# Optimization experiments

Hardware: AMD Instinct MI355X
Metric: run time of the kernel (lower is better)

## Reference

```python
import jax, jax.numpy as jnp
import numpy as np

EPS = 1e-8  # torch F.cosine_similarity eps


def _gather(features, idx):
    # batched_index_select_tensor: per-batch gather along seq dim
    return jnp.take_along_axis(features, idx[:, :, None], axis=1)


def setup_inputs() -> dict:
    key = jax.random.key(0)
    ks = jax.random.split(key, 7)
    B, S, H, Q, D, C = 8, 512, 768, 64, 256, 2
    return {
        "features": jax.random.normal(ks[0], (B, S, H), dtype=jnp.float32),
        "text_a_indices": jax.random.randint(ks[1], (B, Q), 0, S),
        "text_b_indices": jax.random.randint(ks[2], (B, D), 0, S),
        "W1": jax.random.normal(ks[3], (2 * H, H), dtype=jnp.float32) * 0.02,
        "b1": jax.random.normal(ks[4], (H,), dtype=jnp.float32) * 0.02,
        "W2": jax.random.normal(ks[5], (H, C), dtype=jnp.float32) * 0.02,
        "b2": jax.random.normal(ks[6], (C,), dtype=jnp.float32) * 0.02,
    }


def reference(features, text_a_indices, text_b_indices, W1, b1, W2, b2):
    dt = features.dtype
    a_mask = (text_a_indices > 0).astype(dt)          # [B,Q]
    b_mask = (text_b_indices > 0).astype(dt)          # [B,D]
    a_len = jnp.sum(a_mask, axis=-1)                  # [B]
    b_len = jnp.sum(b_mask, axis=-1)                  # [B]

    q_vec = _gather(features, text_a_indices)         # [B,Q,H]
    d_vec = _gather(features, text_b_indices)         # [B,D,H]

    # cosine similarity with torch eps semantics: x.y / (max(|x|,eps)*max(|y|,eps))
    qn = q_vec / jnp.maximum(jnp.linalg.norm(q_vec, axis=-1, keepdims=True), EPS)
    dn = d_vec / jnp.maximum(jnp.linalg.norm(d_vec, axis=-1, keepdims=True), EPS)
    sim = jnp.einsum("bqh,bdh->bqd", qn, dn)          # [B,Q,D]

    # masked weighted average over doc tokens, per query token (fused; no 4D repeat)
    sim_m = sim * b_mask[:, None, :]
    per_q_doc = jnp.einsum("bqd,bdh->bqh", sim_m, d_vec) / b_len[:, None, None]

    # masked average over query tokens
    am = a_mask[:, :, None]
    query_based_doc = jnp.sum(per_q_doc * am, axis=1) / a_len[:, None]   # [B,H]
    query_avg = jnp.sum(q_vec * am, axis=1) / a_len[:, None]             # [B,H]

    feat = jnp.concatenate([query_avg, query_based_doc], axis=-1)        # [B,2H]
    hidden = jax.nn.relu(feat @ W1 + b1)
    logits = hidden @ W2 + b2
    return logits
```

## Files before the change

### kernel.cpp

```cpp
#include <hip/hip_runtime.h>
#include <hip/hip_bf16.h>

#define B_ 8
#define S_ 512
#define H_ 768
#define Q_ 64
#define D_ 256
#define EPSF 1e-8f

#define WS_QBARP  0
#define WS_QAP    (8 * B_ * H_)
#define WS_W      (16 * B_ * H_)
#define WS_HIDDEN (16 * B_ * H_ + B_ * D_)
#define WS_CNT    (WS_HIDDEN + B_ * H_)

__global__ __launch_bounds__(512) void k_qnorm(
        const float* __restrict__ feats,
        const int* __restrict__ aidx,
        float* __restrict__ ws) {
    float* qbar_part = ws + WS_QBARP;
    float* qa_part   = ws + WS_QAP;
    const int b = blockIdx.x >> 3, qg = blockIdx.x & 7;
    const int t = threadIdx.x, wv = t >> 6, lane = t & 63;
    __shared__ int   s_ai[8];
    __shared__ float s_inv[8], s_m[8];
    if (t < 8) s_ai[t] = aidx[b * Q_ + qg * 8 + t];
    __syncthreads();
    {
        int idx = s_ai[wv];
        const float4* row4 = (const float4*)(feats + (size_t)(b * S_ + idx) * H_);
        float4 v0 = row4[lane], v1 = row4[lane + 64], v2 = row4[lane + 128];
        float ss = v0.x*v0.x + v0.y*v0.y + v0.z*v0.z + v0.w*v0.w
                 + v1.x*v1.x + v1.y*v1.y + v1.z*v1.z + v1.w*v1.w
                 + v2.x*v2.x + v2.y*v2.y + v2.z*v2.z + v2.w*v2.w;
        for (int off = 32; off; off >>= 1) ss += __shfl_xor(ss, off, 64);
        if (lane == 0) {
            float inv = 1.f / fmaxf(sqrtf(ss), EPSF);
            s_inv[wv] = (idx > 0) ? inv : 0.f;
            s_m[wv]   = (idx > 0) ? 1.f : 0.f;
        }
    }
    __syncthreads();
    float pb0 = 0.f, pa0 = 0.f, pb1 = 0.f, pa1 = 0.f;
#pragma unroll
    for (int j = 0; j < 8; ++j) {
        const float* row = feats + (size_t)(b * S_ + s_ai[j]) * H_;
        float iv = s_inv[j], mv = s_m[j];
        float f0 = row[t];
        pb0 += f0 * iv; pa0 += f0 * mv;
        if (t < 256) {
            float f1 = row[512 + t];
            pb1 += f1 * iv; pa1 += f1 * mv;
        }
    }
    size_t base = (size_t)(qg * B_ + b) * H_;
    qbar_part[base + t] = pb0;
    qa_part[base + t]   = pa0;
    if (t < 256) {
        qbar_part[base + 512 + t] = pb1;
        qa_part[base + 512 + t]   = pa1;
    }
}

__global__ __launch_bounds__(256) void k_docw(
        const float* __restrict__ feats,
        const int* __restrict__ aidx,
        const int* __restrict__ bidx,
        float* __restrict__ ws) {
    const float* qbar_part = ws + WS_QBARP;
    float* w           = ws + WS_W;
    float* zero_region = ws + WS_HIDDEN;
    const int t = threadIdx.x, wv = t >> 6, lane = t & 63;
    if (blockIdx.x < 25) zero_region[blockIdx.x * 256 + t] = 0.f;
    const int gw = blockIdx.x * 4 + wv;
    const int b = gw >> 8, d = gw & 255;
    __shared__ __align__(16) float s_qbar[H_];
    __shared__ int cnt[4];
    __shared__ float s_alen;
#pragma unroll
    for (int c = 0; c < 3; ++c) {
        int col = c * 256 + t;
        float s = 0.f;
#pragma unroll
        for (int p = 0; p < 8; ++p)
            s += qbar_part[(size_t)(p * B_ + b) * H_ + col];
        s_qbar[col] = s;
    }
    unsigned long long mb = __ballot(bidx[b * D_ + wv * 64 + lane] > 0);
    if (lane == 0) cnt[wv] = __popcll(mb);
    if (wv == 0) {
        unsigned long long ma = __ballot(aidx[b * Q_ + lane] > 0);
        if (lane == 0) s_alen = (float)__popcll(ma);
    }
    __syncthreads();
    float blen = (float)(cnt[0] + cnt[1] + cnt[2] + cnt[3]);
    int idx = bidx[b * D_ + d];
    const float4* row4 = (const float4*)(feats + (size_t)(b * S_ + idx) * H_);
    const float4* q4 = (const float4*)s_qbar;
    float dqf = 0.f, dff = 0.f;
#pragma unroll
    for (int k = 0; k < 3; ++k) {
        float4 v = row4[lane + k * 64];
        float4 q = q4[lane + k * 64];
        dqf += v.x*q.x + v.y*q.y + v.z*q.z + v.w*q.w;
        dff += v.x*v.x + v.y*v.y + v.z*v.z + v.w*v.w;
    }
    for (int off = 32; off; off >>= 1) {
        dqf += __shfl_xor(dqf, off, 64);
        dff += __shfl_xor(dff, off, 64);
    }
    if (lane == 0) {
        float invd = 1.f / fmaxf(sqrtf(dff), EPSF);
        float scale = 1.f / (s_alen * blen);
        w[b * D_ + d] = (idx > 0) ? dqf * invd * scale : 0.f;
    }
}

__global__ __launch_bounds__(256) void k_docsum_mlp(
        const float* __restrict__ feats,
        const int* __restrict__ aidx,
        const int* __restrict__ bidx,
        const float* __restrict__ W1,
        const float* __restrict__ b1,
        const float* __restrict__ W2,
        const float* __restrict__ b2,
        float* __restrict__ ws,
        float* __restrict__ out) {
    const float* qa_part = ws + WS_QAP;
    const float* w       = ws + WS_W;
    float* hidden        = ws + WS_HIDDEN;
    int* counter         = (int*)(ws + WS_CNT);
    const int b = blockIdx.x / 12, hc = blockIdx.x % 12;
    const int t = threadIdx.x, wv = t >> 6, lane = t & 63;
    __shared__ float s_w[D_];
    __shared__ int   s_i[D_];
    __shared__ float s_k[128];
    __shared__ float red[4][64];
    __shared__ float s_alen;
    __shared__ int   s_flag;
    s_w[t] = w[b * D_ + t];
    s_i[t] = bidx[b * D_ + t];
    if (wv == 0) {
        unsigned long long ma = __ballot(aidx[b * Q_ + lane] > 0);
        if (lane == 0) s_alen = (float)__popcll(ma);
    }
    __syncthreads();
    if (t < 64) {
        float s = 0.f;
#pragma unroll
        for (int p = 0; p < 8; ++p)
            s += qa_part[(size_t)(p * B_ + b) * H_ + hc * 64 + t];
        s_k[t] = s / s_alen;
    }
    int hh = hc * 64 + lane;
    float acc = 0.f;
#pragma unroll 8
    for (int d = wv * 64; d < wv * 64 + 64; ++d)
        acc += s_w[d] * feats[(size_t)(b * S_ + s_i[d]) * H_ + hh];
    red[wv][lane] = acc;
    __syncthreads();
    if (t < 64) s_k[64 + t] = red[0][t] + red[1][t] + red[2][t] + red[3][t];
    __syncthreads();
    const float* Wtop = W1 + (size_t)(hc * 64) * H_;
    const float* Wbot = W1 + (size_t)(H_ + hc * 64) * H_;
    float h0 = 0.f, h1 = 0.f, h2 = 0.f;
#pragma unroll 4
    for (int i = 0; i < 64; ++i) {
        float ka = s_k[i], kb = s_k[64 + i];
        const float* r1 = Wtop + (size_t)i * H_;
        const float* r2 = Wbot + (size_t)i * H_;
        h0 += ka * r1[t]       + kb * r2[t];
        h1 += ka * r1[t + 256] + kb * r2[t + 256];
        h2 += ka * r1[t + 512] + kb * r2[t + 512];
    }
    atomicAdd(&hidden[b * H_ + t],       h0);
    atomicAdd(&hidden[b * H_ + t + 256], h1);
    atomicAdd(&hidden[b * H_ + t + 512], h2);
    __threadfence();
    __syncthreads();
    if (t == 0) {
        int old = atomicAdd(counter, 1);
        s_flag = (old == 95);
    }
    __syncthreads();
    if (s_flag) {
        __threadfence();
        for (int bb = wv * 2; bb < wv * 2 + 2; ++bb) {
            float a0 = 0.f, a1 = 0.f;
#pragma unroll
            for (int k = 0; k < 12; ++k) {
                int h = lane + k * 64;
                float hv = __hip_atomic_load(&hidden[bb * H_ + h],
                                             __ATOMIC_RELAXED,
                                             __HIP_MEMORY_SCOPE_AGENT);
                float v = fmaxf(hv + b1[h], 0.f);
                a0 += v * W2[h * 2 + 0];
                a1 += v * W2[h * 2 + 1];
            }
            for (int off = 32; off; off >>= 1) {
                a0 += __shfl_xor(a0, off, 64);
                a1 += __shfl_xor(a1, off, 64);
            }
            if (lane == 0) {
                out[bb * 2 + 0] = a0 + b2[0];
                out[bb * 2 + 1] = a1 + b2[1];
            }
        }
    }
}

extern "C" void kernel_launch(void* const* d_in, const int* in_sizes, int n_in,
                              void* d_out, int out_size, void* d_ws, size_t ws_size,
                              hipStream_t stream) {
    const float* feats = (const float*)d_in[0];
    const int*   aidx  = (const int*)d_in[1];
    const int*   bidx  = (const int*)d_in[2];
    const float* W1    = (const float*)d_in[3];
    const float* b1    = (const float*)d_in[4];
    const float* W2    = (const float*)d_in[5];
    const float* b2    = (const float*)d_in[6];
    float* out = (float*)d_out;
    float* ws = (float*)d_ws;

    k_qnorm<<<64, 512, 0, stream>>>(feats, aidx, ws);
    k_docw<<<512, 256, 0, stream>>>(feats, aidx, bidx, ws);
    k_docsum_mlp<<<96, 256, 0, stream>>>(feats, aidx, bidx, W1, b1, W2, b2, ws, out);
}
```

Before: 101.9 us.

## Fuse doc-weight and doc-sum/MLP kernels with per-batch spin-wait handoff

The separate doc-weight kernel and the doc-sum/MLP kernel become one launch of 608 blocks. The first 512 blocks compute the doc weights and bump a per-batch counter. The last 96 blocks first compute the query-average half of the W1 GEMV, then spin on that counter before doing the weighted doc sum and the second W1 half. The hidden/counter zeroing moves into the first kernel. This removes a kernel boundary and overlaps part of the MLP with the weight computation. The cost is inter-block spinning, which could deadlock if consumer blocks occupied all slots before producers ran.

```diff
diff --git a/kernel.cpp b/kernel.cpp
--- a/kernel.cpp
+++ b/kernel.cpp
@@ -22,6 +22,7 @@
     float* qa_part   = ws + WS_QAP;
     const int b = blockIdx.x >> 3, qg = blockIdx.x & 7;
     const int t = threadIdx.x, wv = t >> 6, lane = t & 63;
+    if (blockIdx.x < 13) ws[WS_HIDDEN + blockIdx.x * 512 + t] = 0.f;
     __shared__ int   s_ai[8];
     __shared__ float s_inv[8], s_m[8];
     if (t < 8) s_ai[t] = aidx[b * Q_ + qg * 8 + t];
@@ -62,61 +63,7 @@
     }
 }
 
-__global__ __launch_bounds__(256) void k_docw(
-        const float* __restrict__ feats,
-        const int* __restrict__ aidx,
-        const int* __restrict__ bidx,
-        float* __restrict__ ws) {
-    const float* qbar_part = ws + WS_QBARP;
-    float* w           = ws + WS_W;
-    float* zero_region = ws + WS_HIDDEN;
-    const int t = threadIdx.x, wv = t >> 6, lane = t & 63;
-    if (blockIdx.x < 25) zero_region[blockIdx.x * 256 + t] = 0.f;
-    const int gw = blockIdx.x * 4 + wv;
-    const int b = gw >> 8, d = gw & 255;
-    __shared__ __align__(16) float s_qbar[H_];
-    __shared__ int cnt[4];
-    __shared__ float s_alen;
-#pragma unroll
-    for (int c = 0; c < 3; ++c) {
-        int col = c * 256 + t;
-        float s = 0.f;
-#pragma unroll
-        for (int p = 0; p < 8; ++p)
-            s += qbar_part[(size_t)(p * B_ + b) * H_ + col];
-        s_qbar[col] = s;
-    }
-    unsigned long long mb = __ballot(bidx[b * D_ + wv * 64 + lane] > 0);
-    if (lane == 0) cnt[wv] = __popcll(mb);
-    if (wv == 0) {
-        unsigned long long ma = __ballot(aidx[b * Q_ + lane] > 0);
-        if (lane == 0) s_alen = (float)__popcll(ma);
-    }
-    __syncthreads();
-    float blen = (float)(cnt[0] + cnt[1] + cnt[2] + cnt[3]);
-    int idx = bidx[b * D_ + d];
-    const float4* row4 = (const float4*)(feats + (size_t)(b * S_ + idx) * H_);
-    const float4* q4 = (const float4*)s_qbar;
-    float dqf = 0.f, dff = 0.f;
-#pragma unroll
-    for (int k = 0; k < 3; ++k) {
-        float4 v = row4[lane + k * 64];
-        float4 q = q4[lane + k * 64];
-        dqf += v.x*q.x + v.y*q.y + v.z*q.z + v.w*q.w;
-        dff += v.x*v.x + v.y*v.y + v.z*v.z + v.w*v.w;
-    }
-    for (int off = 32; off; off >>= 1) {
-        dqf += __shfl_xor(dqf, off, 64);
-        dff += __shfl_xor(dff, off, 64);
-    }
-    if (lane == 0) {
-        float invd = 1.f / fmaxf(sqrtf(dff), EPSF);
-        float scale = 1.f / (s_alen * blen);
-        w[b * D_ + d] = (idx > 0) ? dqf * invd * scale : 0.f;
-    }
-}
-
-__global__ __launch_bounds__(256) void k_docsum_mlp(
+__global__ __launch_bounds__(256) void k_fused2(
         const float* __restrict__ feats,
         const int* __restrict__ aidx,
         const int* __restrict__ bidx,
@@ -126,84 +73,166 @@
         const float* __restrict__ b2,
         float* __restrict__ ws,
         float* __restrict__ out) {
-    const float* qa_part = ws + WS_QAP;
-    const float* w       = ws + WS_W;
-    float* hidden        = ws + WS_HIDDEN;
-    int* counter         = (int*)(ws + WS_CNT);
-    const int b = blockIdx.x / 12, hc = blockIdx.x % 12;
+    const float* qbar_part = ws + WS_QBARP;
+    const float* qa_part   = ws + WS_QAP;
+    float* w       = ws + WS_W;
+    float* hidden  = ws + WS_HIDDEN;
+    int*   wcnt    = (int*)(ws + WS_CNT);
+    int*   gcnt    = wcnt + 8;
+    const int bk = blockIdx.x;
     const int t = threadIdx.x, wv = t >> 6, lane = t & 63;
-    __shared__ float s_w[D_];
-    __shared__ int   s_i[D_];
-    __shared__ float s_k[128];
-    __shared__ float red[4][64];
-    __shared__ float s_alen;
-    __shared__ int   s_flag;
-    s_w[t] = w[b * D_ + t];
-    s_i[t] = bidx[b * D_ + t];
-    if (wv == 0) {
-        unsigned long long ma = __ballot(aidx[b * Q_ + lane] > 0);
-        if (lane == 0) s_alen = (float)__popcll(ma);
-    }
-    __syncthreads();
-    if (t < 64) {
-        float s = 0.f;
-#pragma unroll
-        for (int p = 0; p < 8; ++p)
-            s += qa_part[(size_t)(p * B_ + b) * H_ + hc * 64 + t];
-        s_k[t] = s / s_alen;
-    }
-    int hh = hc * 64 + lane;
-    float acc = 0.f;
+
+    if (bk < 512) {
+        const int gw = bk * 4 + wv;
+        const int b = gw >> 8, d = gw & 255;
+        __shared__ __align__(16) float s_qbar[H_];
+        __shared__ int cnt[4];
+        __shared__ float s_alen;
+#pragma unroll
+        for (int c = 0; c < 3; ++c) {
+            int col = c * 256 + t;
+            float s = 0.f;
+#pragma unroll
+            for (int p = 0; p < 8; ++p)
+                s += qbar_part[(size_t)(p * B_ + b) * H_ + col];
+            s_qbar[col] = s;
+        }
+        unsigned long long mb = __ballot(bidx[b * D_ + wv * 64 + lane] > 0);
+        if (lane == 0) cnt[wv] = __popcll(mb);
+        if (wv == 0) {
+            unsigned long long ma = __ballot(aidx[b * Q_ + lane] > 0);
+            if (lane == 0) s_alen = (float)__popcll(ma);
+        }
+        __syncthreads();
+        float blen = (float)(cnt[0] + cnt[1] + cnt[2] + cnt[3]);
+        int idx = bidx[b * D_ + d];
+        const float4* row4 = (const float4*)(feats + (size_t)(b * S_ + idx) * H_);
+        const float4* q4 = (const float4*)s_qbar;
+        float dqf = 0.f, dff = 0.f;
+#pragma unroll
+        for (int k = 0; k < 3; ++k) {
+            float4 v = row4[lane + k * 64];
+            float4 q = q4[lane + k * 64];
+            dqf += v.x*q.x + v.y*q.y + v.z*q.z + v.w*q.w;
+            dff += v.x*v.x + v.y*v.y + v.z*v.z + v.w*v.w;
+        }
+        for (int off = 32; off; off >>= 1) {
+            dqf += __shfl_xor(dqf, off, 64);
+            dff += __shfl_xor(dff, off, 64);
+        }
+        if (lane == 0) {
+            float invd = 1.f / fmaxf(sqrtf(dff), EPSF);
+            float scale = 1.f / (s_alen * blen);
+            float wd = (idx > 0) ? dqf * invd * scale : 0.f;
+            __hip_atomic_store(&w[b * D_ + d], wd,
+                               __ATOMIC_RELAXED, __HIP_MEMORY_SCOPE_AGENT);
+        }
+        __threadfence();
+        __syncthreads();
+        if (t == 0) atomicAdd(&wcnt[b], 1);
+    } else {
+        const int g = bk - 512;
+        const int b = g / 12, hc = g % 12;
+        __shared__ float s_w[D_];
+        __shared__ int   s_i[D_];
+        __shared__ float s_k[128];
+        __shared__ float red[4][64];
+        __shared__ float s_alen;
+        __shared__ int   s_flag;
+        s_i[t] = bidx[b * D_ + t];
+        if (wv == 0) {
+            unsigned long long ma = __ballot(aidx[b * Q_ + lane] > 0);
+            if (lane == 0) s_alen = (float)__popcll(ma);
+        }
+        __syncthreads();
+        if (t < 64) {
+            float s = 0.f;
+#pragma unroll
+            for (int p = 0; p < 8; ++p)
+                s += qa_part[(size_t)(p * B_ + b) * H_ + hc * 64 + t];
+            s_k[t] = s / s_alen;
+        }
+        __syncthreads();
+        {
+            const float* Wtop = W1 + (size_t)(hc * 64) * H_;
+            float h0 = 0.f, h1 = 0.f, h2 = 0.f;
+#pragma unroll 4
+            for (int i = 0; i < 64; ++i) {
+                float ka = s_k[i];
+                const float* r1 = Wtop + (size_t)i * H_;
+                h0 += ka * r1[t];
+                h1 += ka * r1[t + 256];
+                h2 += ka * r1[t + 512];
+            }
+            atomicAdd(&hidden[b * H_ + t],       h0);
+            atomicAdd(&hidden[b * H_ + t + 256], h1);
+            atomicAdd(&hidden[b * H_ + t + 512], h2);
+        }
+        if (t == 0) {
+            while (__hip_atomic_load(&wcnt[b], __ATOMIC_ACQUIRE,
+                                     __HIP_MEMORY_SCOPE_AGENT) < 64) {
+                __builtin_amdgcn_s_sleep(2);
+            }
+        }
+        __syncthreads();
+        s_w[t] = __hip_atomic_load(&w[b * D_ + t], __ATOMIC_RELAXED,
+                                   __HIP_MEMORY_SCOPE_AGENT);
+        __syncthreads();
+        {
+            int hh = hc * 64 + lane;
+            float acc = 0.f;
 #pragma unroll 8
-    for (int d = wv * 64; d < wv * 64 + 64; ++d)
-        acc += s_w[d] * feats[(size_t)(b * S_ + s_i[d]) * H_ + hh];
-    red[wv][lane] = acc;
-    __syncthreads();
-    if (t < 64) s_k[64 + t] = red[0][t] + red[1][t] + red[2][t] + red[3][t];
-    __syncthreads();
-    const float* Wtop = W1 + (size_t)(hc * 64) * H_;
-    const float* Wbot = W1 + (size_t)(H_ + hc * 64) * H_;
-    float h0 = 0.f, h1 = 0.f, h2 = 0.f;
+            for (int d = wv * 64; d < wv * 64 + 64; ++d)
+                acc += s_w[d] * feats[(size_t)(b * S_ + s_i[d]) * H_ + hh];
+            red[wv][lane] = acc;
+        }
+        __syncthreads();
+        if (t < 64) s_k[64 + t] = red[0][t] + red[1][t] + red[2][t] + red[3][t];
+        __syncthreads();
+        {
+            const float* Wbot = W1 + (size_t)(H_ + hc * 64) * H_;
+            float h0 = 0.f, h1 = 0.f, h2 = 0.f;
 #pragma unroll 4
-    for (int i = 0; i < 64; ++i) {
-        float ka = s_k[i], kb = s_k[64 + i];
-        const float* r1 = Wtop + (size_t)i * H_;
-        const float* r2 = Wbot + (size_t)i * H_;
-        h0 += ka * r1[t]       + kb * r2[t];
-        h1 += ka * r1[t + 256] + kb * r2[t + 256];
-        h2 += ka * r1[t + 512] + kb * r2[t + 512];
-    }
-    atomicAdd(&hidden[b * H_ + t],       h0);
-    atomicAdd(&hidden[b * H_ + t + 256], h1);
-    atomicAdd(&hidden[b * H_ + t + 512], h2);
-    __threadfence();
-    __syncthreads();
-    if (t == 0) {
-        int old = atomicAdd(counter, 1);
-        s_flag = (old == 95);
-    }
-    __syncthreads();
-    if (s_flag) {
+            for (int i = 0; i < 64; ++i) {
+                float kb = s_k[64 + i];
+                const float* r2 = Wbot + (size_t)i * H_;
+                h0 += kb * r2[t];
+                h1 += kb * r2[t + 256];
+                h2 += kb * r2[t + 512];
+            }
+            atomicAdd(&hidden[b * H_ + t],       h0);
+            atomicAdd(&hidden[b * H_ + t + 256], h1);
+            atomicAdd(&hidden[b * H_ + t + 512], h2);
+        }
         __threadfence();
-        for (int bb = wv * 2; bb < wv * 2 + 2; ++bb) {
-            float a0 = 0.f, a1 = 0.f;
-#pragma unroll
-            for (int k = 0; k < 12; ++k) {
-                int h = lane + k * 64;
-                float hv = __hip_atomic_load(&hidden[bb * H_ + h],
-                                             __ATOMIC_RELAXED,
-                                             __HIP_MEMORY_SCOPE_AGENT);
-                float v = fmaxf(hv + b1[h], 0.f);
-                a0 += v * W2[h * 2 + 0];
-                a1 += v * W2[h * 2 + 1];
-            }
-            for (int off = 32; off; off >>= 1) {
-                a0 += __shfl_xor(a0, off, 64);
-                a1 += __shfl_xor(a1, off, 64);
-            }
-            if (lane == 0) {
-                out[bb * 2 + 0] = a0 + b2[0];
-                out[bb * 2 + 1] = a1 + b2[1];
+        __syncthreads();
+        if (t == 0) {
+            int old = atomicAdd(gcnt, 1);
+            s_flag = (old == 95);
+        }
+        __syncthreads();
+        if (s_flag) {
+            __threadfence();
+            for (int bb = wv * 2; bb < wv * 2 + 2; ++bb) {
+                float a0 = 0.f, a1 = 0.f;
+#pragma unroll
+                for (int k = 0; k < 12; ++k) {
+                    int h = lane + k * 64;
+                    float hv = __hip_atomic_load(&hidden[bb * H_ + h],
+                                                 __ATOMIC_RELAXED,
+                                                 __HIP_MEMORY_SCOPE_AGENT);
+                    float v = fmaxf(hv + b1[h], 0.f);
+                    a0 += v * W2[h * 2 + 0];
+                    a1 += v * W2[h * 2 + 1];
+                }
+                for (int off = 32; off; off >>= 1) {
+                    a0 += __shfl_xor(a0, off, 64);
+                    a1 += __shfl_xor(a1, off, 64);
+                }
+                if (lane == 0) {
+                    out[bb * 2 + 0] = a0 + b2[0];
+                    out[bb * 2 + 1] = a1 + b2[1];
+                }
             }
         }
     }
@@ -223,6 +252,5 @@
     float* ws = (float*)d_ws;
 
     k_qnorm<<<64, 512, 0, stream>>>(feats, aidx, ws);
-    k_docw<<<512, 256, 0, stream>>>(feats, aidx, bidx, ws);
-    k_docsum_mlp<<<96, 256, 0, stream>>>(feats, aidx, bidx, W1, b1, W2, b2, ws, out);
+    k_fused2<<<608, 256, 0, stream>>>(feats, aidx, bidx, W1, b1, W2, b2, ws, out);
 }
```

After: 136.6 us. +34.0%, slower.
